# Kernel optimization log

Measured on AMD Instinct MI355X. Metric: run time of the kernel, lower is better.

## Reference

```python
import jax, jax.numpy as jnp
import numpy as np

L = 512          # profile HMM model length (number of match states)
S = 25           # alphabet size (input_dim)
BATCH = 128
T_LEN = 1024
TINY = np.finfo(np.float32).tiny


def setup_inputs():
    key = jax.random.key(0)
    ks = jax.random.split(key, 18)
    def n(k, shape):
        return 0.1 * jax.random.normal(k, shape, dtype=jnp.float32)
    return {
        "seq": jax.random.randint(ks[0], (BATCH, T_LEN), 0, S),
        "em_kernel": n(ks[1], (L, S)),
        "ins_kernel": n(ks[2], (S,)),
        "flank_kernel": n(ks[3], (1,)),
        "btm": n(ks[4], (L,)),
        "m2e": n(ks[5], (L,)),
        "mtm": n(ks[6], (L - 1,)),
        "m2i": n(ks[7], (L - 1,)),
        "i2m": n(ks[8], (L - 1,)),
        "i2i": n(ks[9], (L - 1,)),
        "mtd": n(ks[10], (L,)),
        "dtm": n(ks[11], (L,)),
        "dtd": n(ks[12], (L - 1,)),
        "lf_loop": n(ks[13], (1,)),
        "lf_exit": n(ks[14], (1,)),
        "e2u": n(ks[15], (1,)),
        "e2r": n(ks[16], (1,)),
        "e2t": n(ks[17], (1,)),
    }


def _build_hmm(em_kernel, ins_kernel, flank_kernel, btm, m2e, mtm, m2i, i2m, i2i,
               mtd, dtm, dtd, lf_loop, lf_exit, e2u, e2r, e2t):
    """Build implicit transition matrix A [q,q], emission matrix B [q,S+1], init dist [q].
    Explicit states begin/end/delete are marginalized out (silent states), yielding the
    implicit transition structure of the profile HMM (match skips via delete chains)."""
    Lm = em_kernel.shape[0]
    q = 2 * Lm + 3                      # LF, M_1..M_L, I_1..I_{L-1}, U, RF, T
    U, RF, TM = 2 * Lm, 2 * Lm + 1, 2 * Lm + 2
    idx = jnp.arange(Lm)
    dt = em_kernel.dtype
    # per-source-state softmax over explicit outgoing edges
    begin_p = jax.nn.softmax(jnp.concatenate([btm, mtd[:1]]))            # begin -> M_j / D_1
    btm_p = begin_p[:Lm]
    mp = jax.nn.softmax(jnp.stack([mtm, m2i, m2e[:Lm - 1], mtd[1:]], axis=-1), axis=-1)
    mtm_p, m2i_p, m2e_p, mtd_mid = mp[:, 0], mp[:, 1], mp[:, 2], mp[:, 3]
    ip = jax.nn.softmax(jnp.stack([i2m, i2i], axis=-1), axis=-1)
    i2m_p, i2i_p = ip[:, 0], ip[:, 1]
    dp = jax.nn.softmax(jnp.stack([dtm[:Lm - 1], dtd], axis=-1), axis=-1)
    dtm_p = jnp.concatenate([dp[:, 0], jnp.ones((1,), dt)])              # D_L -> end with prob 1
    dtd_p = dp[:, 1]
    fp = jax.nn.softmax(jnp.concatenate([lf_loop, lf_exit]))            # shared flank kernels
    floop, fexit = fp[0], fp[1]
    ep = jax.nn.softmax(jnp.concatenate([e2u, e2r, e2t]))               # end -> U / RF / T
    # marginalize silent delete chain. Sk[i,k]: P(src_i => target via deletes),
    # src_0 = begin, src_i = M_i; target M_{k+2} for k<=L-2, end for k=L-1.
    mtd_p = jnp.concatenate([begin_p[Lm:], mtd_mid])                    # begin->D_1, M_i->D_{i+1}
    cp_log = jnp.concatenate([jnp.zeros((1,), dt), jnp.cumsum(jnp.log(dtd_p))])
    Sk = mtd_p[:, None] * jnp.exp(cp_log[None, :] - cp_log[:, None]) * dtm_p[None, :]
    Sk = jnp.where(idx[None, :] >= idx[:, None], Sk, jnp.zeros((), dt))
    enter = btm_p + jnp.pad(Sk[0, :Lm - 1], (1, 0))                      # begin => M_j
    begin_end = Sk[0, Lm - 1]                                            # begin => end (all deleted)
    m2e_tot = jnp.concatenate([m2e_p + Sk[1:, Lm - 1], jnp.ones((1,), dt)])
    A = jnp.zeros((q, q), dt)
    Mblk = jnp.zeros((Lm, Lm), dt).at[idx[:-1], idx[1:]].set(mtm_p)
    Mblk = Mblk.at[0:Lm - 1, 1:Lm].add(Sk[1:Lm, 0:Lm - 1])               # match skips (j>=i+2)
    A = A.at[1:Lm + 1, 1:Lm + 1].set(Mblk)
    A = A.at[0, 0].set(floop)
    A = A.at[0, 1:Lm + 1].set(fexit * enter)
    A = A.at[0, U].set(fexit * begin_end * ep[0])
    A = A.at[0, RF].set(fexit * begin_end * ep[1])
    A = A.at[0, TM].set(fexit * begin_end * ep[2])
    A = A.at[jnp.arange(1, Lm), jnp.arange(Lm + 1, 2 * Lm)].set(m2i_p)   # M_i -> I_i
    A = A.at[1:Lm + 1, U].set(m2e_tot * ep[0])
    A = A.at[1:Lm + 1, RF].set(m2e_tot * ep[1])
    A = A.at[1:Lm + 1, TM].set(m2e_tot * ep[2])
    A = A.at[jnp.arange(Lm + 1, 2 * Lm), jnp.arange(2, Lm + 1)].set(i2m_p)  # I_i -> M_{i+1}
    A = A.at[jnp.arange(Lm + 1, 2 * Lm), jnp.arange(Lm + 1, 2 * Lm)].set(i2i_p)
    A = A.at[U, 1:Lm + 1].set(fexit * enter)
    A = A.at[U, U].set(floop + fexit * begin_end * ep[0])
    A = A.at[U, RF].set(fexit * begin_end * ep[1])
    A = A.at[U, TM].set(fexit * begin_end * ep[2])
    A = A.at[RF, RF].set(floop)
    A = A.at[RF, TM].set(fexit)
    A = A.at[TM, TM].set(1.0)
    # emission matrix per make_default_emission_matrix: [ins; em; ins x (L+1)] rows,
    # softmax, zero pad column, terminal one-hot row -> [2L+3, S+1]
    rows = jnp.concatenate([ins_kernel[None], em_kernel,
                            jnp.tile(ins_kernel[None], (Lm + 1, 1))], axis=0)
    Bm = jax.nn.softmax(rows, axis=-1)
    Bm = jnp.concatenate([Bm, jnp.zeros((2 * Lm + 2, 1), dt)], axis=-1)
    s_alph = em_kernel.shape[1]
    Bm = jnp.concatenate([Bm, jax.nn.one_hot(jnp.array([s_alph]), s_alph + 1, dtype=dt)], axis=0)
    # initial distribution: start in left flank w.p. sigmoid(flank_init), else enter model
    p0 = jax.nn.sigmoid(flank_kernel[0])
    init = jnp.zeros((q,), dt).at[0].set(p0)
    init = init.at[1:Lm + 1].set((1 - p0) * enter)
    init = init.at[U].set((1 - p0) * begin_end * ep[0])
    init = init.at[RF].set((1 - p0) * begin_end * ep[1])
    init = init.at[TM].set((1 - p0) * begin_end * ep[2])
    return A, Bm, init


def _forward(seq, *params):
    A, Bm, init = _build_hmm(*params)
    # emission probs per timestep: matvec(B, one_hot(x)) == column gather
    E = Bm.T[seq]                        # [batch, T, q]
    alpha = init[None, :] * E[:, 0]
    s = alpha.sum(-1, keepdims=True) + TINY
    ll = jnp.log(s[:, 0])
    alpha = alpha / s

    def step(carry, Et):
        a, l = carry
        a = Et * (a @ A)                 # forward-algorithm recurrence + scaling
        sn = a.sum(-1, keepdims=True) + TINY
        return (a / sn, l + jnp.log(sn[:, 0])), None

    (alpha, ll), _ = jax.lax.scan(step, (alpha, ll), jnp.swapaxes(E[:, 1:], 0, 1))
    return ll                            # [batch] sequence log-likelihoods


def reference(seq, em_kernel, ins_kernel, flank_kernel, btm, m2e, mtm, m2i, i2m, i2i,
              mtd, dtm, dtd, lf_loop, lf_exit, e2u, e2r, e2t):
    return _forward(seq, em_kernel, ins_kernel, flank_kernel, btm, m2e, mtm, m2i, i2m,
                    i2i, mtd, dtm, dtd, lf_loop, lf_exit, e2u, e2r, e2t)
```

## Files before the change

kernel.cpp:

```cpp
#include <hip/hip_runtime.h>
#include <math.h>

#define LM 512
#define TLEN 1024
#define TINY_F 1.17549435e-38f

#define OFF_ENTER 0
#define OFF_MTM   512
#define OFF_I2M   1024
#define OFF_DTM   1536
#define OFF_WC    2048
#define OFF_MC    2560
#define OFF_M2I   3072
#define OFF_I2I   3584
#define OFF_M2E   4096
#define OFF_INS   4608
#define OFF_SC    4640
#define OFF_EMB   5120

typedef float v2f __attribute__((ext_vector_type(2)));

__device__ __forceinline__ v2f pfma(v2f a, v2f b, v2f c) {
    return __builtin_elementwise_fma(a, b, c);
}
__device__ __forceinline__ v2f vs(float c) { return (v2f){c, c}; }

template<int Ctrl, int RowMask>
__device__ __forceinline__ float fdpp(float oldv, float src) {
    int r = __builtin_amdgcn_update_dpp(
        __builtin_bit_cast(int, oldv), __builtin_bit_cast(int, src),
        Ctrl, RowMask, 0xF, false);
    return __builtin_bit_cast(float, r);
}

template<int Ctrl, int RowMask>
__device__ __forceinline__ float fdppb(float src) {
    int r = __builtin_amdgcn_update_dpp(
        0, __builtin_bit_cast(int, src),
        Ctrl, RowMask, 0xF, true);
    return __builtin_bit_cast(float, r);
}

__device__ __forceinline__ float rdlane63(float v) {
    return __builtin_bit_cast(float,
        __builtin_amdgcn_readlane(__builtin_bit_cast(int, v), 63));
}

__device__ __forceinline__ float wave_sum_to63(float v) {
    v += fdpp<0x111, 0xF>(0.f, v);
    v += fdpp<0x112, 0xF>(0.f, v);
    v += fdpp<0x114, 0xF>(0.f, v);
    v += fdpp<0x118, 0xF>(0.f, v);
    v += fdpp<0x142, 0xA>(0.f, v);
    v += fdpp<0x143, 0xC>(0.f, v);
    return v;
}

__global__ __launch_bounds__(512) void hmm_setup(
    const float* __restrict__ ins,
    const float* __restrict__ flank, const float* __restrict__ btm,
    const float* __restrict__ m2e, const float* __restrict__ mtm,
    const float* __restrict__ m2i, const float* __restrict__ i2m,
    const float* __restrict__ i2i, const float* __restrict__ mtd,
    const float* __restrict__ dtm, const float* __restrict__ dtd,
    const float* __restrict__ lfl, const float* __restrict__ lfe,
    const float* __restrict__ e2u, const float* __restrict__ e2r,
    const float* __restrict__ e2t, float* __restrict__ P)
{
    __shared__ float beginp[513];
    __shared__ float mtdp[512], dtmp[512], dtdp[512], cplog[512];
    __shared__ float mtmp[512], m2ip[512], m2ep[512], i2mp[512], i2ip[512];
    __shared__ float rbuf[512], rbuf2[512];
    const int j = threadIdx.x;

    if (j < 25) {
        float sm = 0.f;
        for (int s = 0; s < 25; ++s) sm += expf(ins[s]);
        P[OFF_INS + j] = log2f(expf(ins[j]) / sm);
    }

    float eb = expf(btm[j]);
    rbuf[j] = eb;
    __syncthreads();
    for (int s = 256; s > 0; s >>= 1) {
        if (j < s) rbuf[j] += rbuf[j + s];
        __syncthreads();
    }
    float e512 = expf(mtd[0]);
    float tot = rbuf[0] + e512;
    beginp[j] = eb / tot;
    if (j == 0) { beginp[512] = e512 / tot; mtdp[0] = e512 / tot; }

    if (j < 511) {
        float a = expf(mtm[j]), b = expf(m2i[j]), c = expf(m2e[j]), d = expf(mtd[j + 1]);
        float s = a + b + c + d;
        mtmp[j] = a / s; m2ip[j] = b / s; m2ep[j] = c / s; mtdp[j + 1] = d / s;
        float ia = expf(i2m[j]), ib = expf(i2i[j]); s = ia + ib;
        i2mp[j] = ia / s; i2ip[j] = ib / s;
        float da = expf(dtm[j]), db = expf(dtd[j]); s = da + db;
        dtmp[j] = da / s; dtdp[j] = db / s;
    }
    if (j == 511) dtmp[511] = 1.0f;
    __syncthreads();

    {
        float lw = (j >= 1) ? logf(dtdp[j - 1]) : 0.f;
        rbuf[j] = lw;
        __syncthreads();
        float* bufs[2] = { rbuf, rbuf2 };
        int cur = 0;
        for (int off = 1; off < 512; off <<= 1) {
            float v = bufs[cur][j];
            if (j >= off) v += bufs[cur][j - off];
            bufs[cur ^ 1][j] = v;
            cur ^= 1;
            __syncthreads();
        }
        cplog[j] = bufs[cur][j];
    }
    __syncthreads();

    if (j == 0) {
        float fl = expf(lfl[0]), fe = expf(lfe[0]); float fs = fl + fe;
        float floop = fl / fs, fexit = fe / fs;
        float eu = expf(e2u[0]), er = expf(e2r[0]), et = expf(e2t[0]);
        float es = eu + er + et; float ep0 = eu / es, ep1 = er / es;
        float p0 = 1.0f / (1.0f + expf(-flank[0]));
        P[OFF_SC + 0] = floop;
        P[OFF_SC + 1] = fexit;
        P[OFF_SC + 2] = p0;
        P[OFF_SC + 5] = ep0;
        P[OFF_SC + 6] = ep1;
        P[OFF_SC + 9] = 1.0f - p0;
    }
    __syncthreads();

    float en = beginp[j];
    if (j >= 1) en += mtdp[0] * expf(cplog[j - 1]) * dtmp[j - 1];
    P[OFF_ENTER + j] = en;
    P[OFF_MTM + j] = (j >= 1) ? mtmp[j - 1] : 0.f;
    P[OFF_I2M + j] = (j >= 1) ? i2mp[j - 1] : 0.f;
    P[OFF_DTM + j] = (j >= 1) ? dtmp[j - 1] : 0.f;
    P[OFF_WC  + j] = (j >= 1) ? mtdp[j]     : 0.f;
    P[OFF_MC  + j] = (j >= 1) ? dtdp[j - 1] : 0.f;
    P[OFF_M2I + j] = (j < 511) ? m2ip[j] : 0.f;
    P[OFF_I2I + j] = (j < 511) ? i2ip[j] : 0.f;
    P[OFF_M2E + j] = (j < 511)
        ? (m2ep[j] + mtdp[j + 1] * expf(cplog[511] - cplog[j + 1]))
        : 1.0f;
}

__global__ __launch_bounds__(64) void hmm_emrel(
    const float* __restrict__ em, const float* __restrict__ ins,
    float* __restrict__ P)
{
    const int j = blockIdx.x * 64 + threadIdx.x;

    float sm = 0.f;
    for (int s = 0; s < 25; ++s) sm += expf(ins[s]);

    const float* row = em + j * 25;
    float mx = row[0];
    for (int s = 1; s < 25; ++s) mx = fmaxf(mx, row[s]);
    float sme = 0.f;
    for (int s = 0; s < 25; ++s) sme += expf(row[s] - mx);
    float inv = 1.0f / sme;

    int lanej = j >> 3, e = j & 7;
    int pos = ((e >> 2) << 8) | (lanej << 2) | (e & 3);
    for (int s = 0; s < 25; ++s) {
        float inspS = expf(ins[s]) / sm;
        P[OFF_EMB + s * 512 + pos] = (expf(row[s] - mx) * inv) / inspS;
    }
}

__global__ __launch_bounds__(64, 1) void hmm_forward(
    const int* __restrict__ seq, const float* __restrict__ P,
    float* __restrict__ out)
{
    __shared__ __align__(16) float sEmb[25 * 512];
    __shared__ float sLogEi[32];
    __shared__ __align__(16) int sSeq[TLEN + 4];

    const int lane = threadIdx.x;
    const int b = blockIdx.x;
    const int base = lane * 8;

    {
        const float4* src = (const float4*)(P + OFF_EMB);
        float4* dst = (float4*)sEmb;
#pragma unroll 5
        for (int k = lane; k < 25 * 128; k += 64) dst[k] = src[k];
        if (lane < 32) sLogEi[lane] = P[OFF_INS + (lane < 25 ? lane : 0)];
        const int4* s4 = (const int4*)(seq + b * TLEN);
        int4* d4 = (int4*)sSeq;
#pragma unroll
        for (int k = lane; k < 256; k += 64) d4[k] = s4[k];
        if (lane < 4) sSeq[TLEN + lane] = 0;
    }
    __syncthreads();

    float llE;
    {
        float le = 0.f;
#pragma unroll
        for (int k = 0; k < 16; ++k) le += sLogEi[sSeq[lane * 16 + k]];
        llE = rdlane63(wave_sum_to63(le));
    }

    float mtm_[8], dtm_[8], wC_[8], mC_[8];
    v2f enter2[4], m2iS2[4], i2i2[4], m2e2[4], dtmM2[4], invNX2[4];
    {
        float enter_[8], m2iS_[8], i2i_[8], m2e_[8], dtmM_[8], invNX_[8];
#pragma unroll
        for (int e = 0; e < 8; ++e) {
            enter_[e] = P[OFF_ENTER + base + e];
            mtm_[e]   = P[OFF_MTM + base + e];
            dtm_[e]   = P[OFF_DTM + base + e];
            wC_[e]    = P[OFF_WC + base + e];
            mC_[e]    = P[OFF_MC + base + e];
            i2i_[e]   = P[OFF_I2I + base + e];
            m2e_[e]   = P[OFF_M2E + base + e];
            float i2mN = (base + e + 1 < 512) ? P[OFF_I2M + base + e + 1] : 1.0f;
            m2iS_[e]  = P[OFF_M2I + base + e] * i2mN;
            invNX_[e] = 1.0f / i2mN;
        }
        float Mp = mC_[0];
        dtmM_[0] = dtm_[0];
#pragma unroll
        for (int e = 1; e < 8; ++e) { dtmM_[e] = dtm_[e] * Mp; Mp *= mC_[e]; }
#pragma unroll
        for (int p = 0; p < 4; ++p) {
            enter2[p] = (v2f){enter_[2*p], enter_[2*p+1]};
            m2iS2[p]  = (v2f){m2iS_[2*p],  m2iS_[2*p+1]};
            i2i2[p]   = (v2f){i2i_[2*p],   i2i_[2*p+1]};
            m2e2[p]   = (v2f){m2e_[2*p],   m2e_[2*p+1]};
            dtmM2[p]  = (v2f){dtmM_[2*p],  dtmM_[2*p+1]};
            invNX2[p] = (v2f){invNX_[2*p], invNX_[2*p+1]};
        }
    }
    const float floop = P[OFF_SC + 0], fexit = P[OFF_SC + 1], p0 = P[OFF_SC + 2];
    const float ep0 = P[OFF_SC + 5], ep1 = P[OFF_SC + 6];
    const float omp0 = P[OFF_SC + 9];
    const v2f floop2 = vs(floop);
    const v2f epv2 = (v2f){ep0, ep1};

    v2f am2[4], ci2[4];
#define AM(e) ((e) & 1 ? am2[(e) >> 1].y : am2[(e) >> 1].x)
#define CI(e) ((e) & 1 ? ci2[(e) >> 1].y : ci2[(e) >> 1].x)

    v2f EmA2[4], EmB2[4];
    {
        int s0 = sSeq[0];
        const float4* c4 = (const float4*)(sEmb + (s0 << 9) + (lane << 2));
        float4 xx = c4[0], yy = c4[64];
        EmA2[0] = (v2f){xx.x, xx.y}; EmA2[1] = (v2f){xx.z, xx.w};
        EmA2[2] = (v2f){yy.x, yy.y}; EmA2[3] = (v2f){yy.z, yy.w};
    }
#pragma unroll
    for (int p = 0; p < 4; ++p) {
        am2[p] = EmA2[p] * vs(omp0) * enter2[p];
        ci2[p] = (v2f){0.f, 0.f};
    }
    v2f GR = (v2f){p0, 0.f};
    float ll2 = llE;

    int symN = sSeq[1];
    {
        const float4* c4 = (const float4*)(sEmb + (symN << 9) + (lane << 2));
        float4 xx = c4[0], yy = c4[64];
        EmA2[0] = (v2f){xx.x, xx.y}; EmA2[1] = (v2f){xx.z, xx.w};
        EmA2[2] = (v2f){yy.x, yy.y}; EmA2[3] = (v2f){yy.z, yy.w};
    }
    symN = sSeq[2];
    int sidx = 3;

#define STEP(EmC2, EmN2, DO_NORM)                                              \
  {                                                                            \
    {                \
      const float4* c4 = (const float4*)(sEmb + (symN << 9) + (lane << 2));    \
      float4 xx = c4[0], yy = c4[64];                                          \
      EmN2[0] = (v2f){xx.x, xx.y}; EmN2[1] = (v2f){xx.z, xx.w};                \
      EmN2[2] = (v2f){yy.x, yy.y}; EmN2[3] = (v2f){yy.z, yy.w};                \
      symN = sSeq[sidx]; ++sidx;                                               \
    }                                                                          \
    float amL = fdppb<0x138, 0xF>(am2[3].y);                                   \
    float ciL = fdppb<0x138, 0xF>(ci2[3].y);                                   \
                 \
    float Apre[8];                                                             \
    Apre[0] = amL * wC_[0];                                                    \
    _Pragma("unroll")                                                          \
    for (int e = 1; e < 8; ++e)                                                \
      Apre[e] = fmaf(Apre[e - 1], mC_[e], AM(e - 1) * wC_[e]);                 \
         \
    float carry = fdppb<0x138, 0xF>(Apre[7]);                                  \
                \
    v2f dv = am2[0] * m2e2[0];                                                 \
    dv = pfma(am2[1], m2e2[1], dv);                                            \
    dv = pfma(am2[2], m2e2[2], dv);                                            \
    dv = pfma(am2[3], m2e2[3], dv);                                            \
    float dsum = rdlane63(wave_sum_to63(dv.x + dv.y));                         \
              \
    float aFU = GR.x * fexit;                                                  \
    GR = pfma(vs(dsum), epv2, GR * floop2);                                    \
       \
    v2f tp[4];                                                                 \
    tp[0].x = fmaf(amL, mtm_[0], ciL);                                         \
    tp[0].y = fmaf(AM(0), mtm_[1], CI(0));                                     \
    tp[1].x = fmaf(AM(1), mtm_[2], CI(1));                                     \
    tp[1].y = fmaf(AM(2), mtm_[3], CI(2));                                     \
    tp[2].x = fmaf(AM(3), mtm_[4], CI(3));                                     \
    tp[2].y = fmaf(AM(4), mtm_[5], CI(4));                                     \
    tp[3].x = fmaf(AM(5), mtm_[6], CI(5));                                     \
    tp[3].y = fmaf(AM(6), mtm_[7], CI(6));                                     \
                       \
    ci2[0] = pfma(am2[0], m2iS2[0], ci2[0] * i2i2[0]);                         \
    ci2[1] = pfma(am2[1], m2iS2[1], ci2[1] * i2i2[1]);                         \
    ci2[2] = pfma(am2[2], m2iS2[2], ci2[2] * i2i2[2]);                         \
    ci2[3] = pfma(am2[3], m2iS2[3], ci2[3] * i2i2[3]);                         \
      \
    v2f aFU2 = vs(aFU), carry2 = vs(carry);                                    \
    tp[0] = pfma(aFU2, enter2[0], tp[0]);                                      \
    tp[1] = pfma(aFU2, enter2[1], tp[1]);                                      \
    tp[2] = pfma(aFU2, enter2[2], tp[2]);                                      \
    tp[3] = pfma(aFU2, enter2[3], tp[3]);                                      \
    tp[0].y = fmaf(dtm_[1], Apre[0], tp[0].y);                                 \
    tp[1].x = fmaf(dtm_[2], Apre[1], tp[1].x);                                 \
    tp[1].y = fmaf(dtm_[3], Apre[2], tp[1].y);                                 \
    tp[2].x = fmaf(dtm_[4], Apre[3], tp[2].x);                                 \
    tp[2].y = fmaf(dtm_[5], Apre[4], tp[2].y);                                 \
    tp[3].x = fmaf(dtm_[6], Apre[5], tp[3].x);                                 \
    tp[3].y = fmaf(dtm_[7], Apre[6], tp[3].y);                                 \
    tp[0] = pfma(dtmM2[0], carry2, tp[0]);                                     \
    tp[1] = pfma(dtmM2[1], carry2, tp[1]);                                     \
    tp[2] = pfma(dtmM2[2], carry2, tp[2]);                                     \
    tp[3] = pfma(dtmM2[3], carry2, tp[3]);                                     \
    am2[0] = EmC2[0] * tp[0];                                                  \
    am2[1] = EmC2[1] * tp[1];                                                  \
    am2[2] = EmC2[2] * tp[2];                                                  \
    am2[3] = EmC2[3] * tp[3];                                                  \
      \
                                      \
    if (DO_NORM) {                                                             \
      v2f ns = pfma(ci2[0], invNX2[0], am2[0]);                                \
      ns += pfma(ci2[1], invNX2[1], am2[1]);                                   \
      ns += pfma(ci2[2], invNX2[2], am2[2]);                                   \
      ns += pfma(ci2[3], invNX2[3], am2[3]);                                   \
      float sl = ns.x + ns.y + ((lane == 0) ? (GR.x + GR.y) : 0.f);            \
      float s = rdlane63(wave_sum_to63(sl)) + TINY_F;                          \
      ll2 += __log2f(s);                                                       \
      float inv = 1.0f / s;                                                    \
      v2f inv2 = vs(inv);                                                      \
      am2[0] *= inv2; am2[1] *= inv2; am2[2] *= inv2; am2[3] *= inv2;          \
      ci2[0] *= inv2; ci2[1] *= inv2; ci2[2] *= inv2; ci2[3] *= inv2;          \
      GR *= inv2;                                                              \
    }                                                                          \
  }

#define PAIR(NORM2)                                                            \
    STEP(EmA2, EmB2, 0)                                                        \
    STEP(EmB2, EmA2, NORM2)

    for (int c = 0; c < 63; ++c) {
        int nf = ((c & 3) == 3);
        PAIR(0) PAIR(0) PAIR(0) PAIR(0)
        PAIR(0) PAIR(0) PAIR(0) PAIR(nf)
    }
    for (int p = 0; p < 7; ++p) {
        PAIR(0)
    }
    STEP(EmA2, EmB2, 1)
#undef PAIR
#undef STEP
#undef AM
#undef CI

    if (lane == 0) out[b] = ll2 * 0.69314718055994530942f;
}

extern "C" void kernel_launch(void* const* d_in, const int* in_sizes, int n_in,
                              void* d_out, int out_size, void* d_ws, size_t ws_size,
                              hipStream_t stream) {
    const int*   seq   = (const int*)d_in[0];
    const float* em    = (const float*)d_in[1];
    const float* ins   = (const float*)d_in[2];
    const float* flank = (const float*)d_in[3];
    const float* btm   = (const float*)d_in[4];
    const float* m2e   = (const float*)d_in[5];
    const float* mtm   = (const float*)d_in[6];
    const float* m2i   = (const float*)d_in[7];
    const float* i2m   = (const float*)d_in[8];
    const float* i2i   = (const float*)d_in[9];
    const float* mtd   = (const float*)d_in[10];
    const float* dtm   = (const float*)d_in[11];
    const float* dtd   = (const float*)d_in[12];
    const float* lfl   = (const float*)d_in[13];
    const float* lfe   = (const float*)d_in[14];
    const float* e2u   = (const float*)d_in[15];
    const float* e2r   = (const float*)d_in[16];
    const float* e2t   = (const float*)d_in[17];
    float* P = (float*)d_ws;
    float* out = (float*)d_out;

    hipLaunchKernelGGL(hmm_emrel, dim3(8), dim3(64), 0, stream, em, ins, P);
    hipLaunchKernelGGL(hmm_setup, dim3(1), dim3(512), 0, stream,
        ins, flank, btm, m2e, mtm, m2i, i2m, i2i, mtd, dtm, dtd,
        lfl, lfe, e2u, e2r, e2t, P);
    hipLaunchKernelGGL(hmm_forward, dim3(128), dim3(64), 0, stream, seq, P, out);
}
```

Measured before the change: 256.7 us.

## Pack eight sequences per 512-thread block sharing one emission table

The forward kernel now runs 8 waves per block, one sequence per wave, so 16 blocks replace 128 single-wave blocks. The 50KB emission table is staged into shared memory once per block rather than once per sequence, and sequences are stored as bytes so that eight fit in LDS. The intent is to cut redundant global-to-LDS loads and per-block setup. The cost is that only 16 CUs are used instead of 128, and the eight waves of a block share one CU's issue slots and LDS bandwidth, which could lengthen the serial per-timestep recurrence.

New measurement: 389.3 us. +51.6%, slower.

```diff
diff --git a/kernel.cpp b/kernel.cpp
--- a/kernel.cpp
+++ b/kernel.cpp
@@ -174,37 +174,43 @@
     }
 }
 
-__global__ __launch_bounds__(64, 1) void hmm_forward(
+__global__ __launch_bounds__(512, 1) void hmm_forward(
     const int* __restrict__ seq, const float* __restrict__ P,
     float* __restrict__ out)
 {
     __shared__ __align__(16) float sEmb[25 * 512];
     __shared__ float sLogEi[32];
-    __shared__ __align__(16) int sSeq[TLEN + 4];
-
-    const int lane = threadIdx.x;
-    const int b = blockIdx.x;
+    __shared__ __align__(4) unsigned char sSeqB[8][TLEN + 8];
+
+    const int tid  = threadIdx.x;
+    const int lane = tid & 63;
+    const int wv   = tid >> 6;
+    const int b    = blockIdx.x * 8 + wv;
     const int base = lane * 8;
 
     {
         const float4* src = (const float4*)(P + OFF_EMB);
         float4* dst = (float4*)sEmb;
-#pragma unroll 5
-        for (int k = lane; k < 25 * 128; k += 64) dst[k] = src[k];
-        if (lane < 32) sLogEi[lane] = P[OFF_INS + (lane < 25 ? lane : 0)];
+        for (int k = tid; k < 25 * 128; k += 512) dst[k] = src[k];
+        if (tid < 32) sLogEi[tid] = P[OFF_INS + (tid < 25 ? tid : 0)];
         const int4* s4 = (const int4*)(seq + b * TLEN);
-        int4* d4 = (int4*)sSeq;
-#pragma unroll
-        for (int k = lane; k < 256; k += 64) d4[k] = s4[k];
-        if (lane < 4) sSeq[TLEN + lane] = 0;
+        unsigned int* drow = (unsigned int*)sSeqB[wv];
+#pragma unroll
+        for (int k = lane; k < 256; k += 64) {
+            int4 v = s4[k];
+            drow[k] = (unsigned)(v.x & 0xff) | ((unsigned)(v.y & 0xff) << 8)
+                    | ((unsigned)(v.z & 0xff) << 16) | ((unsigned)(v.w & 0xff) << 24);
+        }
+        if (lane < 8) sSeqB[wv][TLEN + lane] = 0;
     }
     __syncthreads();
+    const unsigned char* myS = sSeqB[wv];
 
     float llE;
     {
         float le = 0.f;
 #pragma unroll
-        for (int k = 0; k < 16; ++k) le += sLogEi[sSeq[lane * 16 + k]];
+        for (int k = 0; k < 16; ++k) le += sLogEi[myS[lane * 16 + k]];
         llE = rdlane63(wave_sum_to63(le));
     }
 
@@ -251,7 +257,7 @@
 
     v2f EmA2[4], EmB2[4];
     {
-        int s0 = sSeq[0];
+        int s0 = myS[0];
         const float4* c4 = (const float4*)(sEmb + (s0 << 9) + (lane << 2));
         float4 xx = c4[0], yy = c4[64];
         EmA2[0] = (v2f){xx.x, xx.y}; EmA2[1] = (v2f){xx.z, xx.w};
@@ -265,14 +271,14 @@
     v2f GR = (v2f){p0, 0.f};
     float ll2 = llE;
 
-    int symN = sSeq[1];
+    int symN = myS[1];
     {
         const float4* c4 = (const float4*)(sEmb + (symN << 9) + (lane << 2));
         float4 xx = c4[0], yy = c4[64];
         EmA2[0] = (v2f){xx.x, xx.y}; EmA2[1] = (v2f){xx.z, xx.w};
         EmA2[2] = (v2f){yy.x, yy.y}; EmA2[3] = (v2f){yy.z, yy.w};
     }
-    symN = sSeq[2];
+    symN = myS[2];
     int sidx = 3;
 
 #define STEP(EmC2, EmN2, DO_NORM)                                              \
@@ -282,7 +288,7 @@
       float4 xx = c4[0], yy = c4[64];                                          \
       EmN2[0] = (v2f){xx.x, xx.y}; EmN2[1] = (v2f){xx.z, xx.w};                \
       EmN2[2] = (v2f){yy.x, yy.y}; EmN2[3] = (v2f){yy.z, yy.w};                \
-      symN = sSeq[sidx]; ++sidx;                                               \
+      symN = myS[sidx]; ++sidx;                                                \
     }                                                                          \
     float amL = fdppb<0x138, 0xF>(am2[3].y);                                   \
     float ciL = fdppb<0x138, 0xF>(ci2[3].y);                                   \
@@ -406,5 +412,5 @@
     hipLaunchKernelGGL(hmm_setup, dim3(1), dim3(512), 0, stream,
         ins, flank, btm, m2e, mtm, m2i, i2m, i2i, mtd, dtm, dtd,
         lfl, lfe, e2u, e2r, e2t, P);
-    hipLaunchKernelGGL(hmm_forward, dim3(128), dim3(64), 0, stream, seq, P, out);
-}
+    hipLaunchKernelGGL(hmm_forward, dim3(16), dim3(512), 0, stream, seq, P, out);
+}
```

## Interleave two sequences per wave to hide recurrence latency

Applied to the files above, without the earlier changes.

Each 64-lane block now runs the forward recurrence for two batch sequences at once, interleaving their steps so the independent dependency chains can overlap cross-lane DPP and reduction latency. The grid is halved to 64 blocks, and shared memory holds two sequence buffers. This trades fewer active CUs and roughly doubled per-wave instruction count for better latency hiding within each wave. It also raises register pressure.

After: 404.0 us. +57.4%, slower.

```diff
diff --git a/kernel.cpp b/kernel.cpp
--- a/kernel.cpp
+++ b/kernel.cpp
@@ -180,10 +180,12 @@
 {
     __shared__ __align__(16) float sEmb[25 * 512];
     __shared__ float sLogEi[32];
-    __shared__ __align__(16) int sSeq[TLEN + 4];
+    __shared__ __align__(16) int sSeqA[TLEN + 4];
+    __shared__ __align__(16) int sSeqB[TLEN + 4];
 
     const int lane = threadIdx.x;
-    const int b = blockIdx.x;
+    const int bA = blockIdx.x * 2;
+    const int bB = bA + 1;
     const int base = lane * 8;
 
     {
@@ -192,20 +194,28 @@
 #pragma unroll 5
         for (int k = lane; k < 25 * 128; k += 64) dst[k] = src[k];
         if (lane < 32) sLogEi[lane] = P[OFF_INS + (lane < 25 ? lane : 0)];
-        const int4* s4 = (const int4*)(seq + b * TLEN);
-        int4* d4 = (int4*)sSeq;
-#pragma unroll
-        for (int k = lane; k < 256; k += 64) d4[k] = s4[k];
-        if (lane < 4) sSeq[TLEN + lane] = 0;
+        const int4* s4A = (const int4*)(seq + bA * TLEN);
+        const int4* s4B = (const int4*)(seq + bB * TLEN);
+        int4* d4A = (int4*)sSeqA;
+        int4* d4B = (int4*)sSeqB;
+#pragma unroll
+        for (int k = lane; k < 256; k += 64) { d4A[k] = s4A[k]; d4B[k] = s4B[k]; }
+        if (lane < 4) { sSeqA[TLEN + lane] = 0; sSeqB[TLEN + lane] = 0; }
     }
     __syncthreads();
-
-    float llE;
-    {
-        float le = 0.f;
-#pragma unroll
-        for (int k = 0; k < 16; ++k) le += sLogEi[sSeq[lane * 16 + k]];
-        llE = rdlane63(wave_sum_to63(le));
+    const int* mySA = sSeqA;
+    const int* mySB = sSeqB;
+
+    float llEA, llEB;
+    {
+        float leA = 0.f, leB = 0.f;
+#pragma unroll
+        for (int k = 0; k < 16; ++k) {
+            leA += sLogEi[mySA[lane * 16 + k]];
+            leB += sLogEi[mySB[lane * 16 + k]];
+        }
+        llEA = rdlane63(wave_sum_to63(leA));
+        llEB = rdlane63(wave_sum_to63(leB));
     }
 
     float mtm_[8], dtm_[8], wC_[8], mC_[8];
@@ -245,80 +255,96 @@
     const v2f floop2 = vs(floop);
     const v2f epv2 = (v2f){ep0, ep1};
 
-    v2f am2[4], ci2[4];
-#define AM(e) ((e) & 1 ? am2[(e) >> 1].y : am2[(e) >> 1].x)
-#define CI(e) ((e) & 1 ? ci2[(e) >> 1].y : ci2[(e) >> 1].x)
-
-    v2f EmA2[4], EmB2[4];
-    {
-        int s0 = sSeq[0];
+    v2f am2A[4], ci2A[4], am2B[4], ci2B[4];
+#define AMx(ARR, e) ((e) & 1 ? ARR[(e) >> 1].y : ARR[(e) >> 1].x)
+
+    v2f EmPA[4], EmQA[4], EmPB[4], EmQB[4];
+
+    {
+        int s0 = mySA[0];
         const float4* c4 = (const float4*)(sEmb + (s0 << 9) + (lane << 2));
         float4 xx = c4[0], yy = c4[64];
-        EmA2[0] = (v2f){xx.x, xx.y}; EmA2[1] = (v2f){xx.z, xx.w};
-        EmA2[2] = (v2f){yy.x, yy.y}; EmA2[3] = (v2f){yy.z, yy.w};
+        EmPA[0] = (v2f){xx.x, xx.y}; EmPA[1] = (v2f){xx.z, xx.w};
+        EmPA[2] = (v2f){yy.x, yy.y}; EmPA[3] = (v2f){yy.z, yy.w};
+    }
+    {
+        int s0 = mySB[0];
+        const float4* c4 = (const float4*)(sEmb + (s0 << 9) + (lane << 2));
+        float4 xx = c4[0], yy = c4[64];
+        EmPB[0] = (v2f){xx.x, xx.y}; EmPB[1] = (v2f){xx.z, xx.w};
+        EmPB[2] = (v2f){yy.x, yy.y}; EmPB[3] = (v2f){yy.z, yy.w};
     }
 #pragma unroll
     for (int p = 0; p < 4; ++p) {
-        am2[p] = EmA2[p] * vs(omp0) * enter2[p];
-        ci2[p] = (v2f){0.f, 0.f};
-    }
-    v2f GR = (v2f){p0, 0.f};
-    float ll2 = llE;
-
-    int symN = sSeq[1];
-    {
-        const float4* c4 = (const float4*)(sEmb + (symN << 9) + (lane << 2));
+        am2A[p] = EmPA[p] * vs(omp0) * enter2[p];
+        ci2A[p] = (v2f){0.f, 0.f};
+        am2B[p] = EmPB[p] * vs(omp0) * enter2[p];
+        ci2B[p] = (v2f){0.f, 0.f};
+    }
+    v2f GRA = (v2f){p0, 0.f};
+    v2f GRB = (v2f){p0, 0.f};
+    float ll2A = llEA, ll2B = llEB;
+
+    int symNA = mySA[1], symNB = mySB[1];
+    {
+        const float4* c4 = (const float4*)(sEmb + (symNA << 9) + (lane << 2));
         float4 xx = c4[0], yy = c4[64];
-        EmA2[0] = (v2f){xx.x, xx.y}; EmA2[1] = (v2f){xx.z, xx.w};
-        EmA2[2] = (v2f){yy.x, yy.y}; EmA2[3] = (v2f){yy.z, yy.w};
-    }
-    symN = sSeq[2];
-    int sidx = 3;
-
-#define STEP(EmC2, EmN2, DO_NORM)                                              \
+        EmPA[0] = (v2f){xx.x, xx.y}; EmPA[1] = (v2f){xx.z, xx.w};
+        EmPA[2] = (v2f){yy.x, yy.y}; EmPA[3] = (v2f){yy.z, yy.w};
+    }
+    {
+        const float4* c4 = (const float4*)(sEmb + (symNB << 9) + (lane << 2));
+        float4 xx = c4[0], yy = c4[64];
+        EmPB[0] = (v2f){xx.x, xx.y}; EmPB[1] = (v2f){xx.z, xx.w};
+        EmPB[2] = (v2f){yy.x, yy.y}; EmPB[3] = (v2f){yy.z, yy.w};
+    }
+    symNA = mySA[2]; symNB = mySB[2];
+    int sidxA = 3, sidxB = 3;
+
+#define STEP(S, EmC2, EmN2, DO_NORM)                                           \
   {                                                                            \
     {                \
-      const float4* c4 = (const float4*)(sEmb + (symN << 9) + (lane << 2));    \
+      const float4* c4 = (const float4*)(sEmb + (symN##S << 9) + (lane << 2)); \
       float4 xx = c4[0], yy = c4[64];                                          \
       EmN2[0] = (v2f){xx.x, xx.y}; EmN2[1] = (v2f){xx.z, xx.w};                \
       EmN2[2] = (v2f){yy.x, yy.y}; EmN2[3] = (v2f){yy.z, yy.w};                \
-      symN = sSeq[sidx]; ++sidx;                                               \
+      symN##S = myS##S[sidx##S]; ++sidx##S;                                    \
     }                                                                          \
-    float amL = fdppb<0x138, 0xF>(am2[3].y);                                   \
-    float ciL = fdppb<0x138, 0xF>(ci2[3].y);                                   \
+    float amL = fdppb<0x138, 0xF>(am2##S[3].y);                                \
+    float ciL = fdppb<0x138, 0xF>(ci2##S[3].y);                                \
                  \
     float Apre[8];                                                             \
     Apre[0] = amL * wC_[0];                                                    \
     _Pragma("unroll")                                                          \
     for (int e = 1; e < 8; ++e)                                                \
-      Apre[e] = fmaf(Apre[e - 1], mC_[e], AM(e - 1) * wC_[e]);                 \
+      Apre[e] = fmaf(Apre[e - 1], mC_[e], AMx(am2##S, e - 1) * wC_[e]);        \
          \
     float carry = fdppb<0x138, 0xF>(Apre[7]);                                  \
                 \
-    v2f dv = am2[0] * m2e2[0];                                                 \
-    dv = pfma(am2[1], m2e2[1], dv);                                            \
-    dv = pfma(am2[2], m2e2[2], dv);                                            \
-    dv = pfma(am2[3], m2e2[3], dv);                                            \
+    v2f dv = am2##S[0] * m2e2[0];                                              \
+    dv = pfma(am2##S[1], m2e2[1], dv);                                         \
+    dv = pfma(am2##S[2], m2e2[2], dv);                                         \
+    dv = pfma(am2##S[3], m2e2[3], dv);                                         \
     float dsum = rdlane63(wave_sum_to63(dv.x + dv.y));                         \
-              \
-    float aFU = GR.x * fexit;                                                  \
-    GR = pfma(vs(dsum), epv2, GR * floop2);                                    \
-       \
+                       \
+    float aFU = GR##S.x * fexit;                                               \
+    GR##S = pfma(vs(dsum), epv2, GR##S * floop2);                              \
+                                                   \
     v2f tp[4];                                                                 \
     tp[0].x = fmaf(amL, mtm_[0], ciL);                                         \
-    tp[0].y = fmaf(AM(0), mtm_[1], CI(0));                                     \
-    tp[1].x = fmaf(AM(1), mtm_[2], CI(1));                                     \
-    tp[1].y = fmaf(AM(2), mtm_[3], CI(2));                                     \
-    tp[2].x = fmaf(AM(3), mtm_[4], CI(3));                                     \
-    tp[2].y = fmaf(AM(4), mtm_[5], CI(4));                                     \
-    tp[3].x = fmaf(AM(5), mtm_[6], CI(5));                                     \
-    tp[3].y = fmaf(AM(6), mtm_[7], CI(6));                                     \
+    tp[0].y = fmaf(AMx(am2##S, 0), mtm_[1], AMx(ci2##S, 0));                   \
+    tp[1].x = fmaf(AMx(am2##S, 1), mtm_[2], AMx(ci2##S, 1));                   \
+    tp[1].y = fmaf(AMx(am2##S, 2), mtm_[3], AMx(ci2##S, 2));                   \
+    tp[2].x = fmaf(AMx(am2##S, 3), mtm_[4], AMx(ci2##S, 3));                   \
+    tp[2].y = fmaf(AMx(am2##S, 4), mtm_[5], AMx(ci2##S, 4));                   \
+    tp[3].x = fmaf(AMx(am2##S, 5), mtm_[6], AMx(ci2##S, 5));                   \
+    tp[3].y = fmaf(AMx(am2##S, 6), mtm_[7], AMx(ci2##S, 6));                   \
                        \
-    ci2[0] = pfma(am2[0], m2iS2[0], ci2[0] * i2i2[0]);                         \
-    ci2[1] = pfma(am2[1], m2iS2[1], ci2[1] * i2i2[1]);                         \
-    ci2[2] = pfma(am2[2], m2iS2[2], ci2[2] * i2i2[2]);                         \
-    ci2[3] = pfma(am2[3], m2iS2[3], ci2[3] * i2i2[3]);                         \
-      \
+    ci2##S[0] = pfma(am2##S[0], m2iS2[0], ci2##S[0] * i2i2[0]);                \
+    ci2##S[1] = pfma(am2##S[1], m2iS2[1], ci2##S[1] * i2i2[1]);                \
+    ci2##S[2] = pfma(am2##S[2], m2iS2[2], ci2##S[2] * i2i2[2]);                \
+    ci2##S[3] = pfma(am2##S[3], m2iS2[3], ci2##S[3] * i2i2[3]);                \
+                                                             \
     v2f aFU2 = vs(aFU), carry2 = vs(carry);                                    \
     tp[0] = pfma(aFU2, enter2[0], tp[0]);                                      \
     tp[1] = pfma(aFU2, enter2[1], tp[1]);                                      \
@@ -335,31 +361,35 @@
     tp[1] = pfma(dtmM2[1], carry2, tp[1]);                                     \
     tp[2] = pfma(dtmM2[2], carry2, tp[2]);                                     \
     tp[3] = pfma(dtmM2[3], carry2, tp[3]);                                     \
-    am2[0] = EmC2[0] * tp[0];                                                  \
-    am2[1] = EmC2[1] * tp[1];                                                  \
-    am2[2] = EmC2[2] * tp[2];                                                  \
-    am2[3] = EmC2[3] * tp[3];                                                  \
-      \
-                                      \
+    am2##S[0] = EmC2[0] * tp[0];                                               \
+    am2##S[1] = EmC2[1] * tp[1];                                               \
+    am2##S[2] = EmC2[2] * tp[2];                                               \
+    am2##S[3] = EmC2[3] * tp[3];                                               \
     if (DO_NORM) {                                                             \
-      v2f ns = pfma(ci2[0], invNX2[0], am2[0]);                                \
-      ns += pfma(ci2[1], invNX2[1], am2[1]);                                   \
-      ns += pfma(ci2[2], invNX2[2], am2[2]);                                   \
-      ns += pfma(ci2[3], invNX2[3], am2[3]);                                   \
-      float sl = ns.x + ns.y + ((lane == 0) ? (GR.x + GR.y) : 0.f);            \
+      v2f ns = pfma(ci2##S[0], invNX2[0], am2##S[0]);                          \
+      ns += pfma(ci2##S[1], invNX2[1], am2##S[1]);                             \
+      ns += pfma(ci2##S[2], invNX2[2], am2##S[2]);                             \
+      ns += pfma(ci2##S[3], invNX2[3], am2##S[3]);                             \
+      float sl = ns.x + ns.y + ((lane == 0) ? (GR##S.x + GR##S.y) : 0.f);      \
       float s = rdlane63(wave_sum_to63(sl)) + TINY_F;                          \
-      ll2 += __log2f(s);                                                       \
+      ll2##S += __log2f(s);                                                    \
       float inv = 1.0f / s;                                                    \
       v2f inv2 = vs(inv);                                                      \
-      am2[0] *= inv2; am2[1] *= inv2; am2[2] *= inv2; am2[3] *= inv2;          \
-      ci2[0] *= inv2; ci2[1] *= inv2; ci2[2] *= inv2; ci2[3] *= inv2;          \
-      GR *= inv2;                                                              \
+      am2##S[0] *= inv2; am2##S[1] *= inv2;                                    \
+      am2##S[2] *= inv2; am2##S[3] *= inv2;                                    \
+      ci2##S[0] *= inv2; ci2##S[1] *= inv2;                                    \
+      ci2##S[2] *= inv2; ci2##S[3] *= inv2;                                    \
+      GR##S *= inv2;                                                           \
     }                                                                          \
   }
 
+#define DSTEP(EmC, EmN, DO_NORM)                                               \
+    STEP(A, EmC##A, EmN##A, DO_NORM)                                           \
+    STEP(B, EmC##B, EmN##B, DO_NORM)
+
 #define PAIR(NORM2)                                                            \
-    STEP(EmA2, EmB2, 0)                                                        \
-    STEP(EmB2, EmA2, NORM2)
+    DSTEP(EmP, EmQ, 0)                                                         \
+    DSTEP(EmQ, EmP, NORM2)
 
     for (int c = 0; c < 63; ++c) {
         int nf = ((c & 3) == 3);
@@ -369,13 +399,16 @@
     for (int p = 0; p < 7; ++p) {
         PAIR(0)
     }
-    STEP(EmA2, EmB2, 1)
+    DSTEP(EmP, EmQ, 1)
 #undef PAIR
+#undef DSTEP
 #undef STEP
-#undef AM
-#undef CI
-
-    if (lane == 0) out[b] = ll2 * 0.69314718055994530942f;
+#undef AMx
+
+    if (lane == 0) {
+        out[bA] = ll2A * 0.69314718055994530942f;
+        out[bB] = ll2B * 0.69314718055994530942f;
+    }
 }
 
 extern "C" void kernel_launch(void* const* d_in, const int* in_sizes, int n_in,
@@ -406,5 +439,5 @@
     hipLaunchKernelGGL(hmm_setup, dim3(1), dim3(512), 0, stream,
         ins, flank, btm, m2e, mtm, m2i, i2m, i2i, mtd, dtm, dtd,
         lfl, lfe, e2u, e2r, e2t, P);
-    hipLaunchKernelGGL(hmm_forward, dim3(128), dim3(64), 0, stream, seq, P, out);
-}
+    hipLaunchKernelGGL(hmm_forward, dim3(64), dim3(64), 0, stream, seq, P, out);
+}
```
